# Kernel tuning notes

Hardware: AMD Instinct MI355X
Metric: run time of the kernel (lower is better)

## Reference

```python
import jax, jax.numpy as jnp
import numpy as np

B, L, D, H, K = 4, 2048, 1024, 16, 3
HEAD_DIM = D // H
LN_EPS = 1e-5


def setup_inputs() -> dict:
    key = jax.random.key(0)
    ks = jax.random.split(key, 12)
    w = lambda k, shp: jax.random.normal(k, shp, jnp.float32) * (shp[-1] ** -0.5)
    return {
        "x": jax.random.normal(ks[0], (B, L, D), jnp.float32),
        "band_importance": jax.random.normal(ks[1], (1, L), jnp.float32) * 0.02,
        "Wq": w(ks[2], (D, D)), "bq": jnp.zeros((D,), jnp.float32),
        "Wk": w(ks[3], (D, D)), "bk": jnp.zeros((D,), jnp.float32),
        "Wv": w(ks[4], (D, D)), "bv": jnp.zeros((D,), jnp.float32),
        "Wo": w(ks[5], (D, D)), "bo": jnp.zeros((D,), jnp.float32),
        "gamma": jnp.ones((D,), jnp.float32),
        "beta": jnp.zeros((D,), jnp.float32),
    }


def reference(x, band_importance, Wq, bq, Wk, bk, Wv, bv, Wo, bo, gamma, beta):
    Bx, Lx, Dx = x.shape
    hd = Dx // H
    # top-k over softmax(band_importance); PyTorch bool attn_mask: True = BLOCKED
    imp = jax.nn.softmax(band_importance, axis=-1)[0]            # (L,)
    _, idx = jax.lax.top_k(imp, K)                               # (K,) int
    col_mask = jnp.zeros((Lx,), bool).at[idx].set(True)          # (L,) True -> masked out
    bias = jnp.where(col_mask, -jnp.inf, 0.0).astype(x.dtype)    # (L,)

    q = (x @ Wq.T + bq).reshape(Bx, Lx, H, hd)
    k_ = (x @ Wk.T + bk).reshape(Bx, Lx, H, hd)
    v = (x @ Wv.T + bv).reshape(Bx, Lx, H, hd)

    scale = 1.0 / np.sqrt(hd)
    scores = jnp.einsum("bqhd,bkhd->bhqk", q, k_) * scale + bias[None, None, None, :]
    attn = jax.nn.softmax(scores, axis=-1)                       # (B,H,L,L)
    ctx = jnp.einsum("bhqk,bkhd->bqhd", attn, v).reshape(Bx, Lx, Dx)
    attn_out = ctx @ Wo.T + bo

    y = x + attn_out                                             # residual
    mu = jnp.mean(y, axis=-1, keepdims=True)
    var = jnp.mean((y - mu) ** 2, axis=-1, keepdims=True)
    return (y - mu) * jax.lax.rsqrt(var + LN_EPS) * gamma + beta
```

## Files before the change

### kernel.cpp

```cpp
#include <hip/hip_runtime.h>

#define GAS __attribute__((address_space(1)))
#define LAS __attribute__((address_space(3)))

typedef __attribute__((ext_vector_type(8))) short short8;
typedef __attribute__((ext_vector_type(4))) float f32x4;
typedef __attribute__((ext_vector_type(16))) float f32x16;
typedef __attribute__((ext_vector_type(4))) unsigned int u32x4;

#define MFMA16(a,b,c) __builtin_amdgcn_mfma_f32_16x16x32_bf16(a,b,c,0,0,0)
#define MFMA32(a,b,c) __builtin_amdgcn_mfma_f32_32x32x16_bf16(a,b,c,0,0,0)

__device__ __forceinline__ unsigned short f2b(float f) {
  unsigned u = __float_as_uint(f);
  u += 0x7fffu + ((u >> 16) & 1u);
  return (unsigned short)(u >> 16);
}
__device__ __forceinline__ float b2f(unsigned short h) {
  return __uint_as_float(((unsigned)h) << 16);
}
__device__ __forceinline__ unsigned cvtpk(float a, float b) {
  unsigned r;
  asm("v_cvt_pk_bf16_f32 %0, %1, %2" : "=v"(r) : "v"(a), "v"(b));
  return r;
}
__device__ __forceinline__ void pl32swap(unsigned &x, unsigned &y) {
  auto r = __builtin_amdgcn_permlane32_swap((int)x, (int)y, false, false);
  x = (unsigned)r[0]; y = (unsigned)r[1];
}
__device__ __forceinline__ float xhalf_sum(float v) {
  auto r = __builtin_amdgcn_permlane32_swap(__float_as_int(v), __float_as_int(v), false, false);
  return __int_as_float(r[0]) + __int_as_float(r[1]);
}
__device__ __forceinline__ float fexp2(float x) {
  float r;
  asm("v_exp_f32 %0, %1" : "=v"(r) : "v"(x));
  return r;
}

union FW { u32x4 u; short8 s; };

__global__ void cvt_f32_bf16(const float* __restrict__ src,
                             unsigned short* __restrict__ dst, int n4) {
  int i = blockIdx.x * blockDim.x + threadIdx.x;
  if (i >= n4) return;
  float4 v = reinterpret_cast<const float4*>(src)[i];
  ushort4 o;
  o.x = f2b(v.x); o.y = f2b(v.y); o.z = f2b(v.z); o.w = f2b(v.w);
  reinterpret_cast<ushort4*>(dst)[i] = o;
}

__global__ void topk_idx(const float* __restrict__ band, int* __restrict__ idxout) {
  __shared__ float svals[256];
  __shared__ int   sidx[256];
  __shared__ int   chosen[3];
  const int t = threadIdx.x;
  for (int pass = 0; pass < 3; ++pass) {
    float best = -INFINITY; int bi = 1 << 30;
    for (int j = t; j < 2048; j += 256) {
      float v = band[j];
      bool skip = false;
      for (int p2 = 0; p2 < pass; ++p2) skip |= (chosen[p2] == j);
      if (!skip && (v > best || (v == best && j < bi))) { best = v; bi = j; }
    }
    svals[t] = best; sidx[t] = bi;
    __syncthreads();
    for (int s = 128; s > 0; s >>= 1) {
      if (t < s) {
        float v2 = svals[t + s]; int i2 = sidx[t + s];
        if (v2 > svals[t] || (v2 == svals[t] && i2 < sidx[t])) { svals[t] = v2; sidx[t] = i2; }
      }
      __syncthreads();
    }
    if (t == 0) chosen[pass] = sidx[0];
    __syncthreads();
  }
  if (t < 3) idxout[t] = chosen[t];
}

template<int MODE>
__global__ __launch_bounds__(256) void gemm_bt_bias(
    const unsigned short* __restrict__ A,
    const unsigned short* __restrict__ Bw,
    const float* __restrict__ bias,
    unsigned short* __restrict__ C,
    int M, int N, int Kd, float scale)
{
  __shared__ short As[128][64];
  __shared__ short Bs[128][64];
  const int tid = threadIdx.x;
  const int w = tid >> 6, lane = tid & 63;
  const int wm = w >> 1, wn = w & 1;
  const int flat = blockIdx.y * gridDim.x + blockIdx.x;
  const int total = gridDim.x * gridDim.y;
  const int cpx = total >> 3;
  const int swb = (flat & 7) * cpx + (flat >> 3);
  const int m0 = (swb % gridDim.x) * 128, n0 = (swb / gridDim.x) * 128;
  const int rA = lane >> 3, cA = lane & 7;

  f32x4 acc[4][4];
  #pragma unroll
  for (int mt = 0; mt < 4; ++mt)
    #pragma unroll
    for (int nt = 0; nt < 4; ++nt)
      #pragma unroll
      for (int r = 0; r < 4; ++r) acc[mt][nt][r] = 0.f;

  const int nK = Kd >> 6;
  for (int kt = 0; kt < nK; ++kt) {
    #pragma unroll
    for (int j = 0; j < 4; ++j) {
      int r = w * 32 + j * 8;
      const unsigned short* ga = A + (size_t)(m0 + r + rA) * Kd + kt * 64 + cA * 8;
      __builtin_amdgcn_global_load_lds((const GAS void*)ga, (LAS void*)&As[r][0], 16, 0, 0);
      const unsigned short* gb = Bw + (size_t)(n0 + r + rA) * Kd + kt * 64 + cA * 8;
      __builtin_amdgcn_global_load_lds((const GAS void*)gb, (LAS void*)&Bs[r][0], 16, 0, 0);
    }
    __syncthreads();
    #pragma unroll
    for (int kc = 0; kc < 2; ++kc) {
      short8 a[4], b[4];
      #pragma unroll
      for (int mt = 0; mt < 4; ++mt)
        a[mt] = *reinterpret_cast<const short8*>(
            &As[wm * 64 + mt * 16 + (lane & 15)][kc * 32 + (lane >> 4) * 8]);
      #pragma unroll
      for (int nt = 0; nt < 4; ++nt)
        b[nt] = *reinterpret_cast<const short8*>(
            &Bs[wn * 64 + nt * 16 + (lane & 15)][kc * 32 + (lane >> 4) * 8]);
      __builtin_amdgcn_s_setprio(1);
      #pragma unroll
      for (int mt = 0; mt < 4; ++mt)
        #pragma unroll
        for (int nt = 0; nt < 4; ++nt)
          acc[mt][nt] = MFMA16(a[mt], b[nt], acc[mt][nt]);
      __builtin_amdgcn_s_setprio(0);
    }
    __syncthreads();
  }
  #pragma unroll
  for (int nt = 0; nt < 4; ++nt) {
    int col = n0 + wn * 64 + nt * 16 + (lane & 15);
    float bv = bias[col];
    int h_ = col >> 6, d_ = col & 63;
    #pragma unroll
    for (int mt = 0; mt < 4; ++mt) {
      int rbase = m0 + wm * 64 + mt * 16 + ((lane >> 4) << 2);
      #pragma unroll
      for (int r = 0; r < 4; ++r) {
        unsigned short val = f2b((acc[mt][nt][r] + bv) * scale);
        if (MODE == 0) {
          C[(size_t)(rbase + r) * N + col] = val;
        } else {
          int row = rbase + r;
          int b_ = row >> 11, lt_ = row & 2047;
          C[(((size_t)(b_ * 16 + h_)) * 2048 + lt_) * 64 + d_] = val;
        }
      }
    }
  }
}

__global__ __launch_bounds__(256) void transpose_v(
    const unsigned short* __restrict__ vin,
    unsigned short* __restrict__ vout)
{
  __shared__ short T[64 * 64];
  const int lt = blockIdx.x, bh = blockIdx.y;
  const int tid = threadIdx.x;
  #pragma unroll
  for (int p = 0; p < 2; ++p) {
    int id = p * 256 + tid; int l = id >> 3, c = id & 7;
    short8 v = *reinterpret_cast<const short8*>(
        vin + ((size_t)bh * 2048 + lt * 64 + l) * 64 + c * 8);
    *reinterpret_cast<short8*>(&T[l * 64 + ((c ^ (l & 7)) * 8)]) = v;
  }
  __syncthreads();
  #pragma unroll
  for (int p = 0; p < 2; ++p) {
    int id = p * 256 + tid; int d = id >> 3, c2 = id & 7;
    short8 o;
    #pragma unroll
    for (int j = 0; j < 8; ++j) {
      int l = c2 * 8 + j;
      o[j] = T[l * 64 + (((d >> 3) ^ (l & 7)) * 8) + (d & 7)];
    }
    *reinterpret_cast<short8*>(vout + ((size_t)bh * 64 + d) * 2048 + lt * 64 + c2 * 8) = o;
  }
}

#define PACK8(S, j0, OUT) {                                        \
    unsigned A_ = cvtpk(S[(j0)+0], S[(j0)+1]);                     \
    unsigned B_ = cvtpk(S[(j0)+4], S[(j0)+5]);                     \
    unsigned C_ = cvtpk(S[(j0)+2], S[(j0)+3]);                     \
    unsigned D_ = cvtpk(S[(j0)+6], S[(j0)+7]);                     \
    pl32swap(A_, B_); pl32swap(C_, D_);                            \
    FW f_; f_.u[0] = A_; f_.u[1] = C_; f_.u[2] = B_; f_.u[3] = D_; \
    OUT = f_.s; }

__global__ __launch_bounds__(256, 3) void attn3(
    const unsigned short* __restrict__ qg,
    const unsigned short* __restrict__ kg,
    const unsigned short* __restrict__ vtg,
    const int* __restrict__ midx,
    unsigned short* __restrict__ ctx)
{
  __shared__ short Ks[2][64 * 64];
  __shared__ short Vs[2][64 * 64];
  const int tid = threadIdx.x, w = tid >> 6, lane = tid & 63;
  const int flat = blockIdx.y * 16 + blockIdx.x;
  const int swzb = (flat & 7) * 128 + (flat >> 3);
  const int qt = swzb & 15, bh = swzb >> 4;
  const int q0 = qt * 128;
  const int lo5 = lane & 31, hi = lane >> 5;
  const int i0 = midx[0], i1 = midx[1], i2 = midx[2];

  const int qrow = q0 + w * 32 + lo5;
  const unsigned short* qp = qg + ((size_t)bh * 2048 + qrow) * 64 + hi * 8;
  short8 qf[4];
  #pragma unroll
  for (int ds = 0; ds < 4; ++ds) qf[ds] = *reinterpret_cast<const short8*>(qp + ds * 16);

  f32x16 oacc0, oacc1, lacc;
  #pragma unroll
  for (int r = 0; r < 16; ++r) { oacc0[r] = 0.f; oacc1[r] = 0.f; lacc[r] = 0.f; }

  const int swzoff = (((lane & 7) ^ (lane >> 3))) * 8;
  const unsigned short* kp0 =
      kg + ((size_t)bh * 2048 + w * 8 + (lane >> 3)) * 64 + swzoff;
  const unsigned short* kp1 = kp0 + 32 * 64;
  const unsigned short* vp0 =
      vtg + ((size_t)(bh * 64 + w * 8 + (lane >> 3))) * 2048 + swzoff;
  const unsigned short* vp1 = vp0 + 32 * 2048;

#define STAGE3(bufi, tt) do {                                                  \
    __builtin_amdgcn_global_load_lds((const GAS void*)(kp0 + (tt) * 4096),     \
        (LAS void*)&Ks[bufi][(w * 8) * 64], 16, 0, 0);                         \
    __builtin_amdgcn_global_load_lds((const GAS void*)(kp1 + (tt) * 4096),     \
        (LAS void*)&Ks[bufi][(32 + w * 8) * 64], 16, 0, 0);                    \
    __builtin_amdgcn_global_load_lds((const GAS void*)(vp0 + (tt) * 64),       \
        (LAS void*)&Vs[bufi][(w * 8) * 64], 16, 0, 0);                         \
    __builtin_amdgcn_global_load_lds((const GAS void*)(vp1 + (tt) * 64),       \
        (LAS void*)&Vs[bufi][(32 + w * 8) * 64], 16, 0, 0);                    \
  } while (0)

  STAGE3(0, 0);
  __syncthreads();
  int buf = 0;

  for (int t = 0; t < 32; ++t) {
    if (t < 31) STAGE3(buf ^ 1, t + 1);

    f32x16 s0, s1;
    #pragma unroll
    for (int r = 0; r < 16; ++r) { s0[r] = 0.f; s1[r] = 0.f; }
    __builtin_amdgcn_s_setprio(1);
    #pragma unroll
    for (int ds = 0; ds < 4; ++ds) {
      int cw = ds * 2 + hi;
      short8 k0 = *reinterpret_cast<const short8*>(
          &Ks[buf][lo5 * 64 + ((cw ^ (lo5 & 7)) * 8)]);
      short8 k1 = *reinterpret_cast<const short8*>(
          &Ks[buf][(32 + lo5) * 64 + ((cw ^ (lo5 & 7)) * 8)]);
      s0 = MFMA32(k0, qf[ds], s0);
      s1 = MFMA32(k1, qf[ds], s1);
    }
    __builtin_amdgcn_s_setprio(0);

    #pragma unroll
    for (int r = 0; r < 16; ++r) s0[r] = fexp2(s0[r]);
    #pragma unroll
    for (int r = 0; r < 16; ++r) s1[r] = fexp2(s1[r]);

    int t64 = t * 64;
    bool tm = ((unsigned)(i0 - t64) < 64u) | ((unsigned)(i1 - t64) < 64u) |
              ((unsigned)(i2 - t64) < 64u);
    if (tm) {
      #pragma unroll
      for (int r = 0; r < 16; ++r) {
        int kg0 = t64 + (r & 3) + 8 * (r >> 2) + 4 * hi;
        int kg1 = kg0 + 32;
        if (kg0 == i0 || kg0 == i1 || kg0 == i2) s0[r] = 0.f;
        if (kg1 == i0 || kg1 == i1 || kg1 == i2) s1[r] = 0.f;
      }
    }

    #pragma unroll
    for (int r = 0; r < 16; ++r) lacc[r] += s0[r] + s1[r];

    short8 pa[4];
    PACK8(s0, 0, pa[0]); PACK8(s0, 8, pa[1]);
    PACK8(s1, 0, pa[2]); PACK8(s1, 8, pa[3]);

    __builtin_amdgcn_s_setprio(1);
    #pragma unroll
    for (int ks = 0; ks < 4; ++ks) {
      int cw = ks * 2 + hi;
      short8 v0 = *reinterpret_cast<const short8*>(
          &Vs[buf][lo5 * 64 + ((cw ^ (lo5 & 7)) * 8)]);
      short8 v1 = *reinterpret_cast<const short8*>(
          &Vs[buf][(32 + lo5) * 64 + ((cw ^ (lo5 & 7)) * 8)]);
      oacc0 = MFMA32(pa[ks], v0, oacc0);
      oacc1 = MFMA32(pa[ks], v1, oacc1);
    }
    __builtin_amdgcn_s_setprio(0);
    __syncthreads();
    buf ^= 1;
  }

  float lsum = 0.f;
  #pragma unroll
  for (int r = 0; r < 16; ++r) lsum += lacc[r];
  lsum = xhalf_sum(lsum);
  const int bb = bh >> 4, hh = bh & 15;
  float rinv = 1.0f / lsum;
  #pragma unroll
  for (int r = 0; r < 16; ++r) {
    int row = (r & 3) + 8 * (r >> 2) + 4 * hi;
    float rv = __int_as_float(__builtin_amdgcn_ds_bpermute(
        (row + (lane & 32)) * 4, __float_as_int(rinv)));
    int qr = q0 + w * 32 + row;
    size_t base = (((size_t)(bb * 2048 + qr)) * 16 + hh) * 64;
    ctx[base + lo5]      = f2b(oacc0[r] * rv);
    ctx[base + 32 + lo5] = f2b(oacc1[r] * rv);
  }
}

__global__ __launch_bounds__(256) void resid_ln(
    const float* __restrict__ x, const unsigned short* __restrict__ ao,
    const float* __restrict__ gamma, const float* __restrict__ beta,
    float* __restrict__ out)
{
  const int row = blockIdx.x, t = threadIdx.x;
  const size_t base = (size_t)row * 1024;
  float4 xv = reinterpret_cast<const float4*>(x + base)[t];
  ushort4 av = reinterpret_cast<const ushort4*>(ao + base)[t];
  float y[4] = {xv.x + b2f(av.x), xv.y + b2f(av.y), xv.z + b2f(av.z), xv.w + b2f(av.w)};
  float sum = y[0] + y[1] + y[2] + y[3];
  float sq = y[0] * y[0] + y[1] * y[1] + y[2] * y[2] + y[3] * y[3];
  #pragma unroll
  for (int off = 1; off < 64; off <<= 1) {
    sum += __shfl_xor(sum, off);
    sq += __shfl_xor(sq, off);
  }
  __shared__ float s1[4], s2[4];
  int w = t >> 6, lane = t & 63;
  if (lane == 0) { s1[w] = sum; s2[w] = sq; }
  __syncthreads();
  sum = s1[0] + s1[1] + s1[2] + s1[3];
  sq = s2[0] + s2[1] + s2[2] + s2[3];
  float mu = sum * (1.f / 1024.f);
  float var = sq * (1.f / 1024.f) - mu * mu;
  float inv = rsqrtf(var + 1e-5f);
  float4 gv = reinterpret_cast<const float4*>(gamma)[t];
  float4 bv = reinterpret_cast<const float4*>(beta)[t];
  float4 o;
  o.x = (y[0] - mu) * inv * gv.x + bv.x;
  o.y = (y[1] - mu) * inv * gv.y + bv.y;
  o.z = (y[2] - mu) * inv * gv.z + bv.z;
  o.w = (y[3] - mu) * inv * gv.w + bv.w;
  reinterpret_cast<float4*>(out + base)[t] = o;
}

extern "C" void kernel_launch(void* const* d_in, const int* in_sizes, int n_in,
                              void* d_out, int out_size, void* d_ws, size_t ws_size,
                              hipStream_t stream)
{
  const float* x     = (const float*)d_in[0];
  const float* band  = (const float*)d_in[1];
  const float* Wq    = (const float*)d_in[2];
  const float* bq    = (const float*)d_in[3];
  const float* Wk    = (const float*)d_in[4];
  const float* bk    = (const float*)d_in[5];
  const float* Wv    = (const float*)d_in[6];
  const float* bv    = (const float*)d_in[7];
  const float* Wo    = (const float*)d_in[8];
  const float* bo    = (const float*)d_in[9];
  const float* gamma = (const float*)d_in[10];
  const float* beta  = (const float*)d_in[11];
  float* out = (float*)d_out;

  char* ws = (char*)d_ws;
  int*            idxw = (int*)(ws);
  unsigned short* xb   = (unsigned short*)(ws + 4096);
  unsigned short* Wqb  = (unsigned short*)(ws + 16781312);
  unsigned short* Wkb  = (unsigned short*)(ws + 18878464);
  unsigned short* Wvb  = (unsigned short*)(ws + 20975616);
  unsigned short* Wob  = (unsigned short*)(ws + 23072768);
  unsigned short* qb   = (unsigned short*)(ws + 25169920);
  unsigned short* kb   = (unsigned short*)(ws + 41947136);
  unsigned short* vhb  = (unsigned short*)(ws + 58724352);
  unsigned short* vtb  = (unsigned short*)(ws + 75501568);
  unsigned short* ctxb = vhb;
  unsigned short* aob  = qb;

  const float QSCALE = 0.125f * 1.44269504f;

  cvt_f32_bf16<<<8192, 256, 0, stream>>>(x, xb, 2097152);
  cvt_f32_bf16<<<1024, 256, 0, stream>>>(Wq, Wqb, 262144);
  cvt_f32_bf16<<<1024, 256, 0, stream>>>(Wk, Wkb, 262144);
  cvt_f32_bf16<<<1024, 256, 0, stream>>>(Wv, Wvb, 262144);
  cvt_f32_bf16<<<1024, 256, 0, stream>>>(Wo, Wob, 262144);
  topk_idx<<<1, 256, 0, stream>>>(band, idxw);

  gemm_bt_bias<1><<<dim3(64, 8), 256, 0, stream>>>(xb, Wqb, bq, qb, 8192, 1024, 1024, QSCALE);
  gemm_bt_bias<1><<<dim3(64, 8), 256, 0, stream>>>(xb, Wkb, bk, kb, 8192, 1024, 1024, 1.0f);
  gemm_bt_bias<1><<<dim3(64, 8), 256, 0, stream>>>(xb, Wvb, bv, vhb, 8192, 1024, 1024, 1.0f);

  transpose_v<<<dim3(32, 64), 256, 0, stream>>>(vhb, vtb);

  attn3<<<dim3(16, 64), 256, 0, stream>>>(qb, kb, vtb, idxw, ctxb);

  gemm_bt_bias<0><<<dim3(64, 8), 256, 0, stream>>>(ctxb, Wob, bo, aob, 8192, 1024, 1024, 1.0f);

  resid_ln<<<8192, 256, 0, stream>>>(x, aob, gamma, beta, out);
}
```

Baseline: 262.1 us.

## Fuse weight conversions and QKV GEMMs, deepen attention K/V prefetch pipeline

All five fp32-to-bf16 conversions are merged into one launch, and the three Q/K/V projections become a single GEMM over a concatenated weight (grid 64x24), with bias, scale and output pointer chosen per column segment. The attention kernel now prefetches K and V two tiles ahead, issuing K and V loads separately with explicit vmcnt waits and barriers, and loads LDS fragments into registers before the MFMAs. The goal is fewer launches, better occupancy across one larger GEMM grid, and more overlap of global loads with compute. In exchange it adds extra barriers per iteration and more register pressure in attention.

```diff
diff --git a/kernel.cpp b/kernel.cpp
--- a/kernel.cpp
+++ b/kernel.cpp
@@ -40,14 +40,29 @@
 
 union FW { u32x4 u; short8 s; };
 
-__global__ void cvt_f32_bf16(const float* __restrict__ src,
-                             unsigned short* __restrict__ dst, int n4) {
-  int i = blockIdx.x * blockDim.x + threadIdx.x;
-  if (i >= n4) return;
-  float4 v = reinterpret_cast<const float4*>(src)[i];
+__global__ void cvt_all(const float* __restrict__ x,
+                        const float* __restrict__ Wq, const float* __restrict__ Wk,
+                        const float* __restrict__ Wv, const float* __restrict__ Wo,
+                        unsigned short* __restrict__ xb,
+                        unsigned short* __restrict__ Wqkvb,
+                        unsigned short* __restrict__ Wob) {
+  const int bid = blockIdx.x;
+  const float* src;
+  unsigned short* dst;
+  int idx;
+  if (bid < 8192) {
+    src = x; dst = xb; idx = bid * 256 + threadIdx.x;
+  } else {
+    int wb = bid - 8192;
+    int seg = wb >> 10;
+    idx = (wb & 1023) * 256 + threadIdx.x;
+    src = (seg == 0) ? Wq : (seg == 1) ? Wk : (seg == 2) ? Wv : Wo;
+    dst = (seg == 3) ? Wob : (Wqkvb + (size_t)seg * 1048576);
+  }
+  float4 v = reinterpret_cast<const float4*>(src)[idx];
   ushort4 o;
   o.x = f2b(v.x); o.y = f2b(v.y); o.z = f2b(v.z); o.w = f2b(v.w);
-  reinterpret_cast<ushort4*>(dst)[i] = o;
+  reinterpret_cast<ushort4*>(dst)[idx] = o;
 }
 
 __global__ void topk_idx(const float* __restrict__ band, int* __restrict__ idxout) {
@@ -78,26 +93,29 @@
   if (t < 3) idxout[t] = chosen[t];
 }
 
-template<int MODE>
-__global__ __launch_bounds__(256) void gemm_bt_bias(
+__global__ __launch_bounds__(256) void gemm_qkv(
     const unsigned short* __restrict__ A,
-    const unsigned short* __restrict__ Bw,
-    const float* __restrict__ bias,
-    unsigned short* __restrict__ C,
-    int M, int N, int Kd, float scale)
+    const unsigned short* __restrict__ Wqkv,
+    const float* __restrict__ bq, const float* __restrict__ bk,
+    const float* __restrict__ bv,
+    unsigned short* __restrict__ qout, unsigned short* __restrict__ kout,
+    unsigned short* __restrict__ vout, float qscale)
 {
   __shared__ short As[128][64];
   __shared__ short Bs[128][64];
   const int tid = threadIdx.x;
   const int w = tid >> 6, lane = tid & 63;
   const int wm = w >> 1, wn = w & 1;
-  const int flat = blockIdx.y * gridDim.x + blockIdx.x;
-  const int total = gridDim.x * gridDim.y;
-  const int cpx = total >> 3;
-  const int swb = (flat & 7) * cpx + (flat >> 3);
-  const int m0 = (swb % gridDim.x) * 128, n0 = (swb / gridDim.x) * 128;
+  const int flat = blockIdx.y * 64 + blockIdx.x;
+  const int swb = (flat & 7) * 192 + (flat >> 3);
+  const int m0 = (swb & 63) * 128, n0 = (swb >> 6) * 128;
   const int rA = lane >> 3, cA = lane & 7;
 
+  const int seg = n0 >> 10;
+  const float* biasp = (seg == 0) ? bq : (seg == 1) ? bk : bv;
+  unsigned short* outp = (seg == 0) ? qout : (seg == 1) ? kout : vout;
+  const float scale = (seg == 0) ? qscale : 1.0f;
+
   f32x4 acc[4][4];
   #pragma unroll
   for (int mt = 0; mt < 4; ++mt)
@@ -106,14 +124,13 @@
       #pragma unroll
       for (int r = 0; r < 4; ++r) acc[mt][nt][r] = 0.f;
 
-  const int nK = Kd >> 6;
-  for (int kt = 0; kt < nK; ++kt) {
+  for (int kt = 0; kt < 16; ++kt) {
     #pragma unroll
     for (int j = 0; j < 4; ++j) {
       int r = w * 32 + j * 8;
-      const unsigned short* ga = A + (size_t)(m0 + r + rA) * Kd + kt * 64 + cA * 8;
+      const unsigned short* ga = A + (size_t)(m0 + r + rA) * 1024 + kt * 64 + cA * 8;
       __builtin_amdgcn_global_load_lds((const GAS void*)ga, (LAS void*)&As[r][0], 16, 0, 0);
-      const unsigned short* gb = Bw + (size_t)(n0 + r + rA) * Kd + kt * 64 + cA * 8;
+      const unsigned short* gb = Wqkv + (size_t)(n0 + r + rA) * 1024 + kt * 64 + cA * 8;
       __builtin_amdgcn_global_load_lds((const GAS void*)gb, (LAS void*)&Bs[r][0], 16, 0, 0);
     }
     __syncthreads();
@@ -141,22 +158,88 @@
   #pragma unroll
   for (int nt = 0; nt < 4; ++nt) {
     int col = n0 + wn * 64 + nt * 16 + (lane & 15);
-    float bv = bias[col];
-    int h_ = col >> 6, d_ = col & 63;
+    int coll = col & 1023;
+    float bval = biasp[coll];
+    int h_ = coll >> 6, d_ = coll & 63;
     #pragma unroll
     for (int mt = 0; mt < 4; ++mt) {
       int rbase = m0 + wm * 64 + mt * 16 + ((lane >> 4) << 2);
       #pragma unroll
       for (int r = 0; r < 4; ++r) {
-        unsigned short val = f2b((acc[mt][nt][r] + bv) * scale);
-        if (MODE == 0) {
-          C[(size_t)(rbase + r) * N + col] = val;
-        } else {
-          int row = rbase + r;
-          int b_ = row >> 11, lt_ = row & 2047;
-          C[(((size_t)(b_ * 16 + h_)) * 2048 + lt_) * 64 + d_] = val;
-        }
+        unsigned short val = f2b((acc[mt][nt][r] + bval) * scale);
+        int row = rbase + r;
+        int b_ = row >> 11, lt_ = row & 2047;
+        outp[(((size_t)(b_ * 16 + h_)) * 2048 + lt_) * 64 + d_] = val;
       }
+    }
+  }
+}
+
+__global__ __launch_bounds__(256) void gemm_wo(
+    const unsigned short* __restrict__ A,
+    const unsigned short* __restrict__ Bw,
+    const float* __restrict__ bias,
+    unsigned short* __restrict__ C)
+{
+  __shared__ short As[128][64];
+  __shared__ short Bs[128][64];
+  const int tid = threadIdx.x;
+  const int w = tid >> 6, lane = tid & 63;
+  const int wm = w >> 1, wn = w & 1;
+  const int flat = blockIdx.y * 64 + blockIdx.x;
+  const int swb = (flat & 7) * 64 + (flat >> 3);
+  const int m0 = (swb & 63) * 128, n0 = (swb >> 6) * 128;
+  const int rA = lane >> 3, cA = lane & 7;
+
+  f32x4 acc[4][4];
+  #pragma unroll
+  for (int mt = 0; mt < 4; ++mt)
+    #pragma unroll
+    for (int nt = 0; nt < 4; ++nt)
+      #pragma unroll
+      for (int r = 0; r < 4; ++r) acc[mt][nt][r] = 0.f;
+
+  for (int kt = 0; kt < 16; ++kt) {
+    #pragma unroll
+    for (int j = 0; j < 4; ++j) {
+      int r = w * 32 + j * 8;
+      const unsigned short* ga = A + (size_t)(m0 + r + rA) * 1024 + kt * 64 + cA * 8;
+      __builtin_amdgcn_global_load_lds((const GAS void*)ga, (LAS void*)&As[r][0], 16, 0, 0);
+      const unsigned short* gb = Bw + (size_t)(n0 + r + rA) * 1024 + kt * 64 + cA * 8;
+      __builtin_amdgcn_global_load_lds((const GAS void*)gb, (LAS void*)&Bs[r][0], 16, 0, 0);
+    }
+    __syncthreads();
+    #pragma unroll
+    for (int kc = 0; kc < 2; ++kc) {
+      short8 a[4], b[4];
+      #pragma unroll
+      for (int mt = 0; mt < 4; ++mt)
+        a[mt] = *reinterpret_cast<const short8*>(
+            &As[wm * 64 + mt * 16 + (lane & 15)][kc * 32 + (lane >> 4) * 8]);
+      #pragma unroll
+      for (int nt = 0; nt < 4; ++nt)
+        b[nt] = *reinterpret_cast<const short8*>(
+            &Bs[wn * 64 + nt * 16 + (lane & 15)][kc * 32 + (lane >> 4) * 8]);
+      __builtin_amdgcn_s_setprio(1);
+      #pragma unroll
+      for (int mt = 0; mt < 4; ++mt)
+        #pragma unroll
+        for (int nt = 0; nt < 4; ++nt)
+          acc[mt][nt] = MFMA16(a[mt], b[nt], acc[mt][nt]);
+      __builtin_amdgcn_s_setprio(0);
+    }
+    __syncthreads();
+  }
+  #pragma unroll
+  for (int nt = 0; nt < 4; ++nt) {
+    int col = n0 + wn * 64 + nt * 16 + (lane & 15);
+    float bval = bias[col];
+    #pragma unroll
+    for (int mt = 0; mt < 4; ++mt) {
+      int rbase = m0 + wm * 64 + mt * 16 + ((lane >> 4) << 2);
+      #pragma unroll
+      for (int r = 0; r < 4; ++r)
+        C[(size_t)(rbase + r) * 1024 + col] = f2b(acc[mt][nt][r] + bval);
     }
   }
 }
@@ -198,7 +281,7 @@
     FW f_; f_.u[0] = A_; f_.u[1] = C_; f_.u[2] = B_; f_.u[3] = D_; \
     OUT = f_.s; }
 
-__global__ __launch_bounds__(256, 3) void attn3(
+__global__ __launch_bounds__(256, 3) void attn4(
     const unsigned short* __restrict__ qg,
     const unsigned short* __restrict__ kg,
     const unsigned short* __restrict__ vtg,
@@ -233,23 +316,44 @@
       vtg + ((size_t)(bh * 64 + w * 8 + (lane >> 3))) * 2048 + swzoff;
   const unsigned short* vp1 = vp0 + 32 * 2048;
 
-#define STAGE3(bufi, tt) do {                                                  \
+#define STAGE_K(bufi, tt) do {                                                 \
     __builtin_amdgcn_global_load_lds((const GAS void*)(kp0 + (tt) * 4096),     \
         (LAS void*)&Ks[bufi][(w * 8) * 64], 16, 0, 0);                         \
     __builtin_amdgcn_global_load_lds((const GAS void*)(kp1 + (tt) * 4096),     \
         (LAS void*)&Ks[bufi][(32 + w * 8) * 64], 16, 0, 0);                    \
+  } while (0)
+#define STAGE_V(bufi, tt) do {                                                 \
     __builtin_amdgcn_global_load_lds((const GAS void*)(vp0 + (tt) * 64),       \
         (LAS void*)&Vs[bufi][(w * 8) * 64], 16, 0, 0);                         \
     __builtin_amdgcn_global_load_lds((const GAS void*)(vp1 + (tt) * 64),       \
         (LAS void*)&Vs[bufi][(32 + w * 8) * 64], 16, 0, 0);                    \
   } while (0)
 
-  STAGE3(0, 0);
-  __syncthreads();
-  int buf = 0;
+  STAGE_K(0, 0); STAGE_V(0, 0);
+  STAGE_K(1, 1); STAGE_V(1, 1);
 
   for (int t = 0; t < 32; ++t) {
-    if (t < 31) STAGE3(buf ^ 1, t + 1);
+    const int buf = t & 1;
+    if (t < 31) { asm volatile("s_waitcnt vmcnt(4)" ::: "memory"); }
+    else        { asm volatile("s_waitcnt vmcnt(0)" ::: "memory"); }
+    __builtin_amdgcn_sched_barrier(0);
+    __builtin_amdgcn_s_barrier();
+    __builtin_amdgcn_sched_barrier(0);
+
+    short8 kf[8];
+    #pragma unroll
+    for (int ds = 0; ds < 4; ++ds) {
+      int cw = ds * 2 + hi;
+      kf[2 * ds] = *reinterpret_cast<const short8*>(
+          &Ks[buf][lo5 * 64 + ((cw ^ (lo5 & 7)) * 8)]);
+      kf[2 * ds + 1] = *reinterpret_cast<const short8*>(
+          &Ks[buf][(32 + lo5) * 64 + ((cw ^ (lo5 & 7)) * 8)]);
+    }
+    asm volatile("s_waitcnt lgkmcnt(0)" ::: "memory");
+    __builtin_amdgcn_sched_barrier(0);
+    __builtin_amdgcn_s_barrier();
+    __builtin_amdgcn_sched_barrier(0);
+    if (t < 30) STAGE_K(buf, t + 2);
 
     f32x16 s0, s1;
     #pragma unroll
@@ -257,13 +361,8 @@
     __builtin_amdgcn_s_setprio(1);
     #pragma unroll
     for (int ds = 0; ds < 4; ++ds) {
-      int cw = ds * 2 + hi;
-      short8 k0 = *reinterpret_cast<const short8*>(
-          &Ks[buf][lo5 * 64 + ((cw ^ (lo5 & 7)) * 8)]);
-      short8 k1 = *reinterpret_cast<const short8*>(
-          &Ks[buf][(32 + lo5) * 64 + ((cw ^ (lo5 & 7)) * 8)]);
-      s0 = MFMA32(k0, qf[ds], s0);
-      s1 = MFMA32(k1, qf[ds], s1);
+      s0 = MFMA32(kf[2 * ds], qf[ds], s0);
+      s1 = MFMA32(kf[2 * ds + 1], qf[ds], s1);
     }
     __builtin_amdgcn_s_setprio(0);
 
@@ -292,20 +391,28 @@
     PACK8(s0, 0, pa[0]); PACK8(s0, 8, pa[1]);
     PACK8(s1, 0, pa[2]); PACK8(s1, 8, pa[3]);
 
-    __builtin_amdgcn_s_setprio(1);
+    short8 vf[8];
     #pragma unroll
     for (int ks = 0; ks < 4; ++ks) {
       int cw = ks * 2 + hi;
-      short8 v0 = *reinterpret_cast<const short8*>(
+      vf[2 * ks] = *reinterpret_cast<const short8*>(
           &Vs[buf][lo5 * 64 + ((cw ^ (lo5 & 7)) * 8)]);
-      short8 v1 = *reinterpret_cast<const short8*>(
+      vf[2 * ks + 1] = *reinterpret_cast<const short8*>(
           &Vs[buf][(32 + lo5) * 64 + ((cw ^ (lo5 & 7)) * 8)]);
-      oacc0 = MFMA32(pa[ks], v0, oacc0);
-      oacc1 = MFMA32(pa[ks], v1, oacc1);
+    }
+    asm volatile("s_waitcnt lgkmcnt(0)" ::: "memory");
+    __builtin_amdgcn_sched_barrier(0);
+    __builtin_amdgcn_s_barrier();
+    __builtin_amdgcn_sched_barrier(0);
+    if (t < 30) STAGE_V(buf, t + 2);
+
+    __builtin_amdgcn_s_setprio(1);
+    #pragma unroll
+    for (int ks = 0; ks < 4; ++ks) {
+      oacc0 = MFMA32(pa[ks], vf[2 * ks], oacc0);
+      oacc1 = MFMA32(pa[ks], vf[2 * ks + 1], oacc1);
     }
     __builtin_amdgcn_s_setprio(0);
-    __syncthreads();
-    buf ^= 1;
   }
 
   float lsum = 0.f;
@@ -381,37 +488,30 @@
   float* out = (float*)d_out;
 
   char* ws = (char*)d_ws;
-  int*            idxw = (int*)(ws);
-  unsigned short* xb   = (unsigned short*)(ws + 4096);
-  unsigned short* Wqb  = (unsigned short*)(ws + 16781312);
-  unsigned short* Wkb  = (unsigned short*)(ws + 18878464);
-  unsigned short* Wvb  = (unsigned short*)(ws + 20975616);
-  unsigned short* Wob  = (unsigned short*)(ws + 23072768);
-  unsigned short* qb   = (unsigned short*)(ws + 25169920);
-  unsigned short* kb   = (unsigned short*)(ws + 41947136);
-  unsigned short* vhb  = (unsigned short*)(ws + 58724352);
-  unsigned short* vtb  = (unsigned short*)(ws + 75501568);
-  unsigned short* ctxb = vhb;
-  unsigned short* aob  = qb;
+  int*            idxw  = (int*)(ws);
+  unsigned short* xb    = (unsigned short*)(ws + 4096);
+  unsigned short* Wqkvb = (unsigned short*)(ws + 16781312);
+  unsigned short* Wob   = (unsigned short*)(ws + 23072768);
+  unsigned short* qb    = (unsigned short*)(ws + 25169920);
+  unsigned short* kb    = (unsigned short*)(ws + 41947136);
+  unsigned short* vhb   = (unsigned short*)(ws + 58724352);
+  unsigned short* vtb   = (unsigned short*)(ws + 75501568);
+  unsigned short* ctxb  = vhb;
+  unsigned short* aob   = qb;
 
   const float QSCALE = 0.125f * 1.44269504f;
 
-  cvt_f32_bf16<<<8192, 256, 0, stream>>>(x, xb, 2097152);
-  cvt_f32_bf16<<<1024, 256, 0, stream>>>(Wq, Wqb, 262144);
-  cvt_f32_bf16<<<1024, 256, 0, stream>>>(Wk, Wkb, 262144);
-  cvt_f32_bf16<<<1024, 256, 0, stream>>>(Wv, Wvb, 262144);
-  cvt_f32_bf16<<<1024, 256, 0, stream>>>(Wo, Wob, 262144);
+  cvt_all<<<12288, 256, 0, stream>>>(x, Wq, Wk, Wv, Wo, xb, Wqkvb, Wob);
   topk_idx<<<1, 256, 0, stream>>>(band, idxw);
 
-  gemm_bt_bias<1><<<dim3(64, 8), 256, 0, stream>>>(xb, Wqb, bq, qb, 8192, 1024, 1024, QSCALE);
-  gemm_bt_bias<1><<<dim3(64, 8), 256, 0, stream>>>(xb, Wkb, bk, kb, 8192, 1024, 1024, 1.0f);
-  gemm_bt_bias<1><<<dim3(64, 8), 256, 0, stream>>>(xb, Wvb, bv, vhb, 8192, 1024, 1024, 1.0f);
+  gemm_qkv<<<dim3(64, 24), 256, 0, stream>>>(xb, Wqkvb, bq, bk, bv,
+                                             qb, kb, vhb, QSCALE);
 
   transpose_v<<<dim3(32, 64), 256, 0, stream>>>(vhb, vtb);
 
-  attn3<<<dim3(16, 64), 256, 0, stream>>>(qb, kb, vtb, idxw, ctxb);
-
-  gemm_bt_bias<0><<<dim3(64, 8), 256, 0, stream>>>(ctxb, Wob, bo, aob, 8192, 1024, 1024, 1.0f);
+  attn4<<<dim3(16, 64), 256, 0, stream>>>(qb, kb, vtb, idxw, ctxb);
+
+  gemm_wo<<<dim3(64, 8), 256, 0, stream>>>(ctxb, Wob, bo, aob);
 
   resid_ln<<<8192, 256, 0, stream>>>(x, aob, gamma, beta, out);
 }
```

New measurement: 232.4 us. -11.3%, faster.
